# Optimization experiments

Hardware: AMD Instinct MI355X
Metric: run time of the kernel (lower is better)

## Reference

```python
import jax, jax.numpy as jnp
import numpy as np

ALLOWED_SPANLEN = 7
NEG = -10000.0      # init value for logalpha, matching torch fill_(-10000.)
MASK_NEG = -1e9     # additive mask for out-of-window span starts


def setup_inputs() -> dict:
    key = jax.random.key(0)
    k1, k2 = jax.random.split(key)
    B, L, T = 16, 128, 11  # batch, sent_len, tagset_size (9 tags + START + STOP)
    scores = jax.random.normal(k1, (B, L, L, T, T), dtype=jnp.float32)
    # mask holds sentence lengths in [L//2, L] (used as gather index into logalpha)
    mask = jax.random.randint(k2, (B,), L // 2, L + 1, dtype=jnp.int32)
    return {"scores": scores, "mask": mask}


def reference(scores, mask):
    """Semi-CRF forward DP (get_logloss_denominator).

    scores: (B, L, L, T, T) -- scores[b, j, i, y_prev, y] is the score of a span
            [j, i] labeled y, with previous segment label y_prev.
    mask:   (B,) sentence lengths.
    """
    B, L, _, T, _ = scores.shape
    K = ALLOWED_SPANLEN
    start_id, stop_id = T - 1, T - 2

    alpha0 = jnp.full((B, L + 1, T), NEG, dtype=scores.dtype)
    alpha0 = alpha0.at[:, 0, start_id].set(0.0)

    # Re-index scores by span-end position so scan can stream one end per step.
    scores_by_end = jnp.moveaxis(scores, 2, 0)  # (L_end, B, L_start, T, T)
    offs = jnp.arange(K)

    def step(alpha, xs):
        i, sc = xs                # i in [1..L]; sc: (B, L, Tprev, Tcur), end = i-1
        js = i - K + offs         # candidate span starts: [i-K, i-1]
        valid = (js >= 0)[None, :, None, None]
        jsc = jnp.clip(js, 0, L - 1)
        a_w = jnp.take(alpha, jsc, axis=1)   # (B, K, Tprev)
        s_w = jnp.take(sc, jsc, axis=1)      # (B, K, Tprev, Tcur)
        t = jnp.where(valid, s_w + a_w[:, :, :, None], MASK_NEG)
        new = jax.nn.logsumexp(t, axis=(1, 2))           # (B, Tcur)
        alpha = jax.lax.dynamic_update_slice(alpha, new[:, None, :], (0, i, 0))
        return alpha, None

    alpha, _ = jax.lax.scan(step, alpha0, (jnp.arange(1, L + 1), scores_by_end))
    # gather logalpha at the sentence-length position for each batch element
    final = alpha[jnp.arange(B), mask, :]                # (B, T)
    return final[:, stop_id].sum()
```

## Files before the change

kernel.cpp:

```cpp
#include <hip/hip_runtime.h>
#include <math.h>

#define LL 128
#define TT 11
#define NP 121
#define KK 7
#define GS 20
#define SPW 240

#define LOG2E 1.4426950408889634f
#define LN2   0.6931471805599453f

__device__ __forceinline__ float fast_exp2(float x) { return __builtin_amdgcn_exp2f(x); }
__device__ __forceinline__ float fast_log2(float x) { return __builtin_amdgcn_logf(x); }
#if __has_builtin(__builtin_amdgcn_rcpf)
__device__ __forceinline__ float fast_rcp(float x) { return __builtin_amdgcn_rcpf(x); }
#else
__device__ __forceinline__ float fast_rcp(float x) { return 1.0f / x; }
#endif
__device__ __forceinline__ float rfl(float x) {
    return __int_as_float(__builtin_amdgcn_readfirstlane(__float_as_int(x)));
}
__device__ __forceinline__ void cfence() { __builtin_amdgcn_wave_barrier(); }

__global__ __launch_bounds__(64, 1) void hscrf_fused(const float* __restrict__ scores,
                                                     const int* __restrict__ mask,
                                                     float* __restrict__ out,
                                                     int n_batch)
{
    const int l = threadIdx.x;
    const int b = blockIdx.x;
    if (b >= n_batch) return;

    __shared__ __align__(64) float sp[SPW];

    const int o1  = l + 64;
    const int o1c = (o1 < NP) ? o1 : 0;
    const int y0 = l / TT,   yp0 = l % TT;
    const int y1 = o1c / TT, yp1 = o1c % TT;
    const int e0 = yp0 * TT + y0;
    const int e1 = yp1 * TT + y1;
    const int i0w = y0 * GS + yp0;
    const int i1w = (o1 < NP) ? (y1 * GS + yp1) : (220 + (l - 57));

    if (l < TT) sp[l * GS + 11] = 0.0f;

    const int mb = mask[b];
    const float* sb = scores + (size_t)b * (size_t)(LL * LL * NP);

    float rA0[KK], rA1[KK], rB0[KK], rB1[KK];
    float rC0[KK], rC1[KK], rD0[KK], rD1[KK];
    float eX0[KK], eX1[KK], eY0[KK], eY1[KK];

    auto load_pane = [&](int p, float (&L0)[KK], float (&L1)[KK]) {
#pragma unroll
        for (int k = 0; k < KK; ++k) {
            const int j  = p - KK + k;
            const int jc = j < 0 ? 0 : j;
            const size_t base = ((size_t)jc * LL + (size_t)(p - 1)) * NP;
            L0[k] = sb[base + e0];
            L1[k] = sb[base + e1];
        }
    };

    auto convert = [&](int p, const float (&R0)[KK], const float (&R1)[KK],
                       float (&D0)[KK], float (&D1)[KK]) {
#pragma unroll
        for (int k = 0; k < KK; ++k) {
            const float ev0 = fast_exp2(R0[k] * LOG2E);
            const float ev1 = fast_exp2(R1[k] * LOG2E);
            const bool ok = (p - KK + k) >= 0;
            D0[k] = ok ? ev0 : 0.0f;
            D1[k] = ok ? ev1 : 0.0f;
        }
    };

    float W0[KK], W1[KK];
#pragma unroll
    for (int k = 0; k < KK; ++k) { W0[k] = 0.0f; W1[k] = 0.0f; }
    W0[KK - 1] = (yp0 == TT - 1) ? 1.0f : 0.0f;
    W1[KK - 1] = (yp1 == TT - 1) ? 1.0f : 0.0f;

    float Cc = 0.0f;
    float saved = 0.0f;

    load_pane(1, rA0, rA1); load_pane(2, rB0, rB1);
    load_pane(3, rC0, rC1); load_pane(4, rD0, rD1);
    convert(1, rA0, rA1, eX0, eX1);
    convert(2, rB0, rB1, eY0, eY1);

    auto body = [&](int i, bool do_load, bool do_conv,
                    float (&EC0)[KK], float (&EC1)[KK],
                    float (&LT0)[KK], float (&LT1)[KK],
                    float (&RS0)[KK], float (&RS1)[KK]) {
        float p0 = fmaf(EC0[0], W0[0], EC0[1] * W0[1]);
        float q0 = fmaf(EC0[2], W0[2], EC0[3] * W0[3]);
        float u0 = fmaf(EC0[4], W0[4], EC0[5] * W0[5]);
        float s0 = (p0 + q0) + fmaf(EC0[6], W0[6], u0);
        float p1 = fmaf(EC1[0], W1[0], EC1[1] * W1[1]);
        float q1 = fmaf(EC1[2], W1[2], EC1[3] * W1[3]);
        float u1 = fmaf(EC1[4], W1[4], EC1[5] * W1[5]);
        float s1 = (p1 + q1) + fmaf(EC1[6], W1[6], u1);
        sp[i0w] = s0;
        sp[i1w] = s1;

        cfence();

        const float4 qa0 = *(const float4*)(sp + yp0 * GS);
        const float4 qb0 = *(const float4*)(sp + yp0 * GS + 4);
        const float4 qc0 = *(const float4*)(sp + yp0 * GS + 8);
        const float4 qa1 = *(const float4*)(sp + yp1 * GS);
        const float4 qb1 = *(const float4*)(sp + yp1 * GS + 4);
        const float4 qc1 = *(const float4*)(sp + yp1 * GS + 8);

        if (do_load) load_pane(i + 4, LT0, LT1);
        if (do_conv) convert(i + 2, RS0, RS1, EC0, EC1);

        const float SA = (((qa0.x + qa0.y) + (qa0.z + qa0.w)) +
                          ((qb0.x + qb0.y) + (qb0.z + qb0.w))) +
                         ((qc0.x + qc0.y) + (qc0.z + qc0.w));
        const float SB = (((qa1.x + qa1.y) + (qa1.z + qa1.w)) +
                          ((qb1.x + qb1.y) + (qb1.z + qb1.w))) +
                         ((qc1.x + qc1.y) + (qc1.z + qc1.w));

        const float s0u = rfl(SA);
        const float r = fast_rcp(s0u);

        saved = (i == mb) ? Cc + fast_log2(SA) : saved;
        Cc += fast_log2(s0u);

#pragma unroll
        for (int k = 0; k < KK - 1; ++k) { W0[k] = W0[k + 1] * r; W1[k] = W1[k + 1] * r; }
        W0[KK - 1] = SA * r;
        W1[KK - 1] = SB * r;

        cfence();
    };

    for (int i = 1; i <= LL - 4; i += 4) {
        body(i,     true, true, eX0, eX1, rA0, rA1, rC0, rC1);
        body(i + 1, true, true, eY0, eY1, rB0, rB1, rD0, rD1);
        body(i + 2, true, true, eX0, eX1, rC0, rC1, rA0, rA1);
        body(i + 3, true, true, eY0, eY1, rD0, rD1, rB0, rB1);
    }
    body(LL - 3, false, true,  eX0, eX1, rA0, rA1, rC0, rC1);
    body(LL - 2, false, true,  eY0, eY1, rB0, rB1, rD0, rD1);
    body(LL - 1, false, false, eX0, eX1, rA0, rA1, rA0, rA1);
    body(LL,     false, false, eY0, eY1, rB0, rB1, rB0, rB1);

    if (l == TT - 2) {
        atomicAdd(out, saved * LN2);
    }
}

extern "C" void kernel_launch(void* const* d_in, const int* in_sizes, int n_in,
                              void* d_out, int out_size, void* d_ws, size_t ws_size,
                              hipStream_t stream) {
    const float* scores = (const float*)d_in[0];
    const int*   mask   = (const int*)d_in[1];
    float* out = (float*)d_out;
    const int B = in_sizes[1];

    hipMemsetAsync(out, 0, sizeof(float) * out_size, stream);

    (void)d_ws; (void)ws_size;

    hscrf_fused<<<B, 64, 0, stream>>>(scores, mask, out, B);
}
```

Before: 210.4 us.

## Stream score panes into an LDS ring via async global-to-LDS loads

New measurement: 248.0 us. +17.9%, slower.

```diff
diff --git a/kernel.cpp b/kernel.cpp
--- a/kernel.cpp
+++ b/kernel.cpp
@@ -7,9 +7,13 @@
 #define KK 7
 #define GS 20
 #define SPW 240
+#define NSLOT 8
 
 #define LOG2E 1.4426950408889634f
 #define LN2   0.6931471805599453f
+
+typedef const __attribute__((address_space(1))) unsigned int* gas_t;
+typedef __attribute__((address_space(3)))       unsigned int* las_t;
 
 __device__ __forceinline__ float fast_exp2(float x) { return __builtin_amdgcn_exp2f(x); }
 __device__ __forceinline__ float fast_log2(float x) { return __builtin_amdgcn_logf(x); }
@@ -23,15 +27,27 @@
 }
 __device__ __forceinline__ void cfence() { __builtin_amdgcn_wave_barrier(); }
 
-__global__ __launch_bounds__(64, 1) void hscrf_fused(const float* __restrict__ scores,
-                                                     const int* __restrict__ mask,
-                                                     float* __restrict__ out,
-                                                     int n_batch)
+__device__ __forceinline__ void vmwait(int n) {
+    switch (n) {
+        case 0:  asm volatile("s_waitcnt vmcnt(0)"  ::: "memory"); break;
+        case 7:  asm volatile("s_waitcnt vmcnt(7)"  ::: "memory"); break;
+        case 14: asm volatile("s_waitcnt vmcnt(14)" ::: "memory"); break;
+        case 21: asm volatile("s_waitcnt vmcnt(21)" ::: "memory"); break;
+        case 28: asm volatile("s_waitcnt vmcnt(28)" ::: "memory"); break;
+        default: break;
+    }
+}
+
+__global__ __launch_bounds__(64, 1) void hscrf_fused2(const float* __restrict__ scores,
+                                                      const int* __restrict__ mask,
+                                                      float* __restrict__ out,
+                                                      int n_batch)
 {
     const int l = threadIdx.x;
     const int b = blockIdx.x;
     if (b >= n_batch) return;
 
+    __shared__ __align__(64) float ring[NSLOT][KK][256];
     __shared__ __align__(64) float sp[SPW];
 
     const int o1  = l + 64;
@@ -39,39 +55,44 @@
     const int y0 = l / TT,   yp0 = l % TT;
     const int y1 = o1c / TT, yp1 = o1c % TT;
     const int e0 = yp0 * TT + y0;
-    const int e1 = yp1 * TT + y1;
+    const int e1 = o1c % TT * TT + o1c / TT;
+    const int f0 = e0;
+    const int f1 = (e1 == 120) ? 123 : e1;
     const int i0w = y0 * GS + yp0;
     const int i1w = (o1 < NP) ? (y1 * GS + yp1) : (220 + (l - 57));
 
     if (l < TT) sp[l * GS + 11] = 0.0f;
 
     const int mb = mask[b];
-    const float* sb = scores + (size_t)b * (size_t)(LL * LL * NP);
+    const float* sb = scores + (size_t)b * (size_t)(LL * (size_t)LL * NP);
 
-    float rA0[KK], rA1[KK], rB0[KK], rB1[KK];
-    float rC0[KK], rC1[KK], rD0[KK], rD1[KK];
-    float eX0[KK], eX1[KK], eY0[KK], eY1[KK];
+    const int src_off = (l < 30) ? l * 16 : ((l == 30) ? 468 : 0);
 
-    auto load_pane = [&](int p, float (&L0)[KK], float (&L1)[KK]) {
+    auto dma_pane = [&](int p) {
+        const int slot = p & (NSLOT - 1);
+        const int pi = p - 1;
 #pragma unroll
         for (int k = 0; k < KK; ++k) {
             const int j  = p - KK + k;
             const int jc = j < 0 ? 0 : j;
-            const size_t base = ((size_t)jc * LL + (size_t)(p - 1)) * NP;
-            L0[k] = sb[base + e0];
-            L1[k] = sb[base + e1];
+            const float* slice = sb + ((size_t)jc * LL + (size_t)pi) * NP;
+            __builtin_amdgcn_global_load_lds(
+                (gas_t)((const char*)slice + src_off),
+                (las_t)&ring[slot][k][0], 16, 0, 0);
         }
     };
 
-    auto convert = [&](int p, const float (&R0)[KK], const float (&R1)[KK],
-                       float (&D0)[KK], float (&D1)[KK]) {
+    auto convert = [&](int p, float (&D0)[KK], float (&D1)[KK]) {
+        const int slot = p & (NSLOT - 1);
 #pragma unroll
         for (int k = 0; k < KK; ++k) {
-            const float ev0 = fast_exp2(R0[k] * LOG2E);
-            const float ev1 = fast_exp2(R1[k] * LOG2E);
+            const float r0 = ring[slot][k][f0];
+            const float r1 = ring[slot][k][f1];
+            const float v0 = fast_exp2(r0 * LOG2E);
+            const float v1 = fast_exp2(r1 * LOG2E);
             const bool ok = (p - KK + k) >= 0;
-            D0[k] = ok ? ev0 : 0.0f;
-            D1[k] = ok ? ev1 : 0.0f;
+            D0[k] = ok ? v0 : 0.0f;
+            D1[k] = ok ? v1 : 0.0f;
         }
     };
 
@@ -84,15 +105,15 @@
     float Cc = 0.0f;
     float saved = 0.0f;
 
-    load_pane(1, rA0, rA1); load_pane(2, rB0, rB1);
-    load_pane(3, rC0, rC1); load_pane(4, rD0, rD1);
-    convert(1, rA0, rA1, eX0, eX1);
-    convert(2, rB0, rB1, eY0, eY1);
+    float eX0[KK], eX1[KK], eY0[KK], eY1[KK];
 
-    auto body = [&](int i, bool do_load, bool do_conv,
+    dma_pane(1); dma_pane(2); dma_pane(3); dma_pane(4); dma_pane(5);
+    vmwait(28);
+    convert(1, eX0, eX1);
+
+    auto body = [&](int i, bool do_load, int vmw, bool do_conv,
                     float (&EC0)[KK], float (&EC1)[KK],
-                    float (&LT0)[KK], float (&LT1)[KK],
-                    float (&RS0)[KK], float (&RS1)[KK]) {
+                    float (&EN0)[KK], float (&EN1)[KK]) {
         float p0 = fmaf(EC0[0], W0[0], EC0[1] * W0[1]);
         float q0 = fmaf(EC0[2], W0[2], EC0[3] * W0[3]);
         float u0 = fmaf(EC0[4], W0[4], EC0[5] * W0[5]);
@@ -113,8 +134,9 @@
         const float4 qb1 = *(const float4*)(sp + yp1 * GS + 4);
         const float4 qc1 = *(const float4*)(sp + yp1 * GS + 8);
 
-        if (do_load) load_pane(i + 4, LT0, LT1);
-        if (do_conv) convert(i + 2, RS0, RS1, EC0, EC1);
+        if (do_load) dma_pane(i + 5);
+        vmwait(vmw);
+        if (do_conv) convert(i + 1, EN0, EN1);
 
         const float SA = (((qa0.x + qa0.y) + (qa0.z + qa0.w)) +
                           ((qb0.x + qb0.y) + (qb0.z + qb0.w))) +
@@ -137,16 +159,16 @@
         cfence();
     };
 
-    for (int i = 1; i <= LL - 4; i += 4) {
-        body(i,     true, true, eX0, eX1, rA0, rA1, rC0, rC1);
-        body(i + 1, true, true, eY0, eY1, rB0, rB1, rD0, rD1);
-        body(i + 2, true, true, eX0, eX1, rC0, rC1, rA0, rA1);
-        body(i + 3, true, true, eY0, eY1, rD0, rD1, rB0, rB1);
+    for (int i = 1; i <= 121; i += 2) {
+        body(i,     true, 28, true, eX0, eX1, eY0, eY1);
+        body(i + 1, true, 28, true, eY0, eY1, eX0, eX1);
     }
-    body(LL - 3, false, true,  eX0, eX1, rA0, rA1, rC0, rC1);
-    body(LL - 2, false, true,  eY0, eY1, rB0, rB1, rD0, rD1);
-    body(LL - 1, false, false, eX0, eX1, rA0, rA1, rA0, rA1);
-    body(LL,     false, false, eY0, eY1, rB0, rB1, rB0, rB1);
+    body(123, true,  28, true,  eX0, eX1, eY0, eY1);
+    body(124, false, 21, true,  eY0, eY1, eX0, eX1);
+    body(125, false, 14, true,  eX0, eX1, eY0, eY1);
+    body(126, false,  7, true,  eY0, eY1, eX0, eX1);
+    body(127, false,  0, true,  eX0, eX1, eY0, eY1);
+    body(128, false, -1, false, eY0, eY1, eX0, eX1);
 
     if (l == TT - 2) {
         atomicAdd(out, saved * LN2);
@@ -165,5 +187,5 @@
 
     (void)d_ws; (void)ws_size;
 
-    hscrf_fused<<<B, 64, 0, stream>>>(scores, mask, out, B);
+    hscrf_fused2<<<B, 64, 0, stream>>>(scores, mask, out, B);
 }
```

## Split loading and DP into producer/consumer waves with an LDS ring buffer

Applied to the files above, without the earlier changes.

Measured after the change: 200.7 us. -4.6%, faster.

```diff
diff --git a/kernel.cpp b/kernel.cpp
--- a/kernel.cpp
+++ b/kernel.cpp
@@ -7,6 +7,8 @@
 #define KK 7
 #define GS 20
 #define SPW 240
+#define NSLOT 8
+#define PANEF 1024
 
 #define LOG2E 1.4426950408889634f
 #define LN2   0.6931471805599453f
@@ -22,134 +24,190 @@
     return __int_as_float(__builtin_amdgcn_readfirstlane(__float_as_int(x)));
 }
 __device__ __forceinline__ void cfence() { __builtin_amdgcn_wave_barrier(); }
-
-__global__ __launch_bounds__(64, 1) void hscrf_fused(const float* __restrict__ scores,
-                                                     const int* __restrict__ mask,
-                                                     float* __restrict__ out,
-                                                     int n_batch)
+#define VMWAIT28() asm volatile("s_waitcnt vmcnt(28)" ::: "memory")
+#define VMWAIT0()  asm volatile("s_waitcnt vmcnt(0)"  ::: "memory")
+#define LGKM0()    asm volatile("s_waitcnt lgkmcnt(0)" ::: "memory")
+
+__device__ __forceinline__ void block_sync() {
+    asm volatile("" ::: "memory");
+    __builtin_amdgcn_s_barrier();
+    asm volatile("" ::: "memory");
+}
+
+__global__ __launch_bounds__(128, 1) void hscrf_pc(const float* __restrict__ scores,
+                                                   const int* __restrict__ mask,
+                                                   float* __restrict__ out,
+                                                   int n_batch)
 {
-    const int l = threadIdx.x;
-    const int b = blockIdx.x;
+    const int tid = threadIdx.x;
+    const int l   = tid & 63;
+    const int wid = tid >> 6;
+    const int b   = blockIdx.x;
     if (b >= n_batch) return;
 
+    __shared__ __align__(64) float ring[NSLOT][PANEF];
     __shared__ __align__(64) float sp[SPW];
 
-    const int o1  = l + 64;
-    const int o1c = (o1 < NP) ? o1 : 0;
-    const int y0 = l / TT,   yp0 = l % TT;
-    const int y1 = o1c / TT, yp1 = o1c % TT;
-    const int e0 = yp0 * TT + y0;
-    const int e1 = yp1 * TT + y1;
-    const int i0w = y0 * GS + yp0;
-    const int i1w = (o1 < NP) ? (y1 * GS + yp1) : (220 + (l - 57));
-
-    if (l < TT) sp[l * GS + 11] = 0.0f;
-
-    const int mb = mask[b];
-    const float* sb = scores + (size_t)b * (size_t)(LL * LL * NP);
-
-    float rA0[KK], rA1[KK], rB0[KK], rB1[KK];
-    float rC0[KK], rC1[KK], rD0[KK], rD1[KK];
-    float eX0[KK], eX1[KK], eY0[KK], eY1[KK];
-
-    auto load_pane = [&](int p, float (&L0)[KK], float (&L1)[KK]) {
-#pragma unroll
-        for (int k = 0; k < KK; ++k) {
-            const int j  = p - KK + k;
-            const int jc = j < 0 ? 0 : j;
-            const size_t base = ((size_t)jc * LL + (size_t)(p - 1)) * NP;
-            L0[k] = sb[base + e0];
-            L1[k] = sb[base + e1];
+    const float* sb = scores + (size_t)b * (size_t)(LL * (size_t)LL * NP);
+
+    if (wid == 1) {
+        const int o1  = l + 64;
+        const bool v1 = (o1 < NP);
+        const int o1c = v1 ? o1 : 0;
+        const int e0 = (l % TT) * TT + (l / TT);
+        const int e1 = (o1c % TT) * TT + (o1c / TT);
+
+        float XA0[KK], XA1[KK], XB0[KK], XB1[KK];
+        float YA0[KK], YA1[KK], YB0[KK], YB1[KK];
+
+        auto issue2 = [&](int p, float (&a0)[KK], float (&a1)[KK],
+                          float (&c0)[KK], float (&c1)[KK]) {
+#pragma unroll
+            for (int k = 0; k < KK; ++k) {
+                const int j = p - KK + k; const int jc = j < 0 ? 0 : j;
+                const float* s0 = sb + ((size_t)jc * LL + (size_t)(p - 1)) * NP;
+                a0[k] = s0[e0]; a1[k] = s0[e1];
+            }
+#pragma unroll
+            for (int k = 0; k < KK; ++k) {
+                const int j = p + 1 - KK + k; const int jc = j < 0 ? 0 : j;
+                const float* s1 = sb + ((size_t)jc * LL + (size_t)p) * NP;
+                c0[k] = s1[e0]; c1[k] = s1[e1];
+            }
+        };
+
+        auto conv1 = [&](int p, const float (&a0)[KK], const float (&a1)[KK]) {
+            const int slot = p & (NSLOT - 1);
+            float v0[8], v1[8];
+#pragma unroll
+            for (int k = 0; k < KK; ++k) {
+                const bool ok = (p - KK + k) >= 0;
+                const float t0 = fast_exp2(a0[k] * LOG2E);
+                const float t1 = fast_exp2(a1[k] * LOG2E);
+                v0[k] = ok ? t0 : 0.0f;
+                v1[k] = (ok && v1) ? t1 : 0.0f;
+            }
+            v0[7] = 0.0f; v1[7] = 0.0f;
+            float4* dst = (float4*)&ring[slot][0];
+            dst[l]       = make_float4(v0[0], v0[1], v0[2], v0[3]);
+            dst[128 + l] = make_float4(v0[4], v0[5], v0[6], v0[7]);
+            dst[64 + l]  = make_float4(v1[0], v1[1], v1[2], v1[3]);
+            dst[192 + l] = make_float4(v1[4], v1[5], v1[6], v1[7]);
+        };
+
+        issue2(1, XA0, XA1, XB0, XB1);
+        issue2(3, YA0, YA1, YB0, YB1);
+        VMWAIT28();
+        conv1(1, XA0, XA1); conv1(2, XB0, XB1);
+        issue2(5, XA0, XA1, XB0, XB1);
+        VMWAIT28();
+        conv1(3, YA0, YA1); conv1(4, YB0, YB1);
+        LGKM0(); block_sync();
+
+        for (int t = 1; t <= 59; t += 2) {
+            issue2(2 * t + 5, YA0, YA1, YB0, YB1);
+            VMWAIT28();
+            conv1(2 * t + 3, XA0, XA1); conv1(2 * t + 4, XB0, XB1);
+            LGKM0(); block_sync();
+            issue2(2 * t + 7, XA0, XA1, XB0, XB1);
+            VMWAIT28();
+            conv1(2 * t + 5, YA0, YA1); conv1(2 * t + 6, YB0, YB1);
+            LGKM0(); block_sync();
         }
-    };
-
-    auto convert = [&](int p, const float (&R0)[KK], const float (&R1)[KK],
-                       float (&D0)[KK], float (&D1)[KK]) {
-#pragma unroll
-        for (int k = 0; k < KK; ++k) {
-            const float ev0 = fast_exp2(R0[k] * LOG2E);
-            const float ev1 = fast_exp2(R1[k] * LOG2E);
-            const bool ok = (p - KK + k) >= 0;
-            D0[k] = ok ? ev0 : 0.0f;
-            D1[k] = ok ? ev1 : 0.0f;
+        issue2(127, YA0, YA1, YB0, YB1);
+        VMWAIT28();
+        conv1(125, XA0, XA1); conv1(126, XB0, XB1);
+        LGKM0(); block_sync();
+        VMWAIT0();
+        conv1(127, YA0, YA1); conv1(128, YB0, YB1);
+        LGKM0(); block_sync();
+        block_sync();
+        block_sync();
+    } else {
+        const int o1  = l + 64;
+        const int o1c = (o1 < NP) ? o1 : 0;
+        const int y0 = l / TT,   yp0 = l % TT;
+        const int y1 = o1c / TT, yp1 = o1c % TT;
+        const int i0w = y0 * GS + yp0;
+        const int i1w = (o1 < NP) ? (y1 * GS + yp1) : (220 + (l - 57));
+
+        if (l < TT) sp[l * GS + 11] = 0.0f;
+
+        const int mb = mask[b];
+
+        float W0[KK], W1[KK];
+#pragma unroll
+        for (int k = 0; k < KK; ++k) { W0[k] = 0.0f; W1[k] = 0.0f; }
+        W0[KK - 1] = (yp0 == TT - 1) ? 1.0f : 0.0f;
+        W1[KK - 1] = (yp1 == TT - 1) ? 1.0f : 0.0f;
+
+        float Cc = 0.0f;
+        float saved = 0.0f;
+
+        block_sync();
+
+        const float4* ep1 = (const float4*)&ring[1][0];
+        float4 ea0 = ep1[l],      ea1 = ep1[128 + l];
+        float4 eb0 = ep1[64 + l], eb1 = ep1[192 + l];
+
+        auto body = [&](int i) {
+            float p0 = fmaf(ea0.x, W0[0], ea0.y * W0[1]);
+            float q0 = fmaf(ea0.z, W0[2], ea0.w * W0[3]);
+            float u0 = fmaf(ea1.x, W0[4], ea1.y * W0[5]);
+            float s0 = (p0 + q0) + fmaf(ea1.z, W0[6], u0);
+            float p1 = fmaf(eb0.x, W1[0], eb0.y * W1[1]);
+            float q1 = fmaf(eb0.z, W1[2], eb0.w * W1[3]);
+            float u1 = fmaf(eb1.x, W1[4], eb1.y * W1[5]);
+            float s1 = (p1 + q1) + fmaf(eb1.z, W1[6], u1);
+            sp[i0w] = s0;
+            sp[i1w] = s1;
+
+            cfence();
+
+            const float4 qa0 = *(const float4*)(sp + yp0 * GS);
+            const float4 qb0 = *(const float4*)(sp + yp0 * GS + 4);
+            const float4 qc0 = *(const float4*)(sp + yp0 * GS + 8);
+            const float4 qa1 = *(const float4*)(sp + yp1 * GS);
+            const float4 qb1 = *(const float4*)(sp + yp1 * GS + 4);
+            const float4 qc1 = *(const float4*)(sp + yp1 * GS + 8);
+
+            const int ns = (i + 1) & (NSLOT - 1);
+            const float4* ep = (const float4*)&ring[ns][0];
+            const float4 na0 = ep[l],      na1 = ep[128 + l];
+            const float4 nb0 = ep[64 + l], nb1 = ep[192 + l];
+
+            const float SA = (((qa0.x + qa0.y) + (qa0.z + qa0.w)) +
+                              ((qb0.x + qb0.y) + (qb0.z + qb0.w))) +
+                             ((qc0.x + qc0.y) + (qc0.z + qc0.w));
+            const float SB = (((qa1.x + qa1.y) + (qa1.z + qa1.w)) +
+                              ((qb1.x + qb1.y) + (qb1.z + qb1.w))) +
+                             ((qc1.x + qc1.y) + (qc1.z + qc1.w));
+
+            const float s0u = rfl(SA);
+            const float r = fast_rcp(s0u);
+
+            saved = (i == mb) ? Cc + fast_log2(SA) : saved;
+            Cc += fast_log2(s0u);
+
+#pragma unroll
+            for (int k = 0; k < KK - 1; ++k) { W0[k] = W0[k + 1] * r; W1[k] = W1[k + 1] * r; }
+            W0[KK - 1] = SA * r;
+            W1[KK - 1] = SB * r;
+
+            ea0 = na0; ea1 = na1; eb0 = nb0; eb1 = nb1;
+
+            cfence();
+        };
+
+        for (int i = 1; i <= LL; i += 2) {
+            body(i);
+            body(i + 1);
+            block_sync();
         }
-    };
-
-    float W0[KK], W1[KK];
-#pragma unroll
-    for (int k = 0; k < KK; ++k) { W0[k] = 0.0f; W1[k] = 0.0f; }
-    W0[KK - 1] = (yp0 == TT - 1) ? 1.0f : 0.0f;
-    W1[KK - 1] = (yp1 == TT - 1) ? 1.0f : 0.0f;
-
-    float Cc = 0.0f;
-    float saved = 0.0f;
-
-    load_pane(1, rA0, rA1); load_pane(2, rB0, rB1);
-    load_pane(3, rC0, rC1); load_pane(4, rD0, rD1);
-    convert(1, rA0, rA1, eX0, eX1);
-    convert(2, rB0, rB1, eY0, eY1);
-
-    auto body = [&](int i, bool do_load, bool do_conv,
-                    float (&EC0)[KK], float (&EC1)[KK],
-                    float (&LT0)[KK], float (&LT1)[KK],
-                    float (&RS0)[KK], float (&RS1)[KK]) {
-        float p0 = fmaf(EC0[0], W0[0], EC0[1] * W0[1]);
-        float q0 = fmaf(EC0[2], W0[2], EC0[3] * W0[3]);
-        float u0 = fmaf(EC0[4], W0[4], EC0[5] * W0[5]);
-        float s0 = (p0 + q0) + fmaf(EC0[6], W0[6], u0);
-        float p1 = fmaf(EC1[0], W1[0], EC1[1] * W1[1]);
-        float q1 = fmaf(EC1[2], W1[2], EC1[3] * W1[3]);
-        float u1 = fmaf(EC1[4], W1[4], EC1[5] * W1[5]);
-        float s1 = (p1 + q1) + fmaf(EC1[6], W1[6], u1);
-        sp[i0w] = s0;
-        sp[i1w] = s1;
-
-        cfence();
-
-        const float4 qa0 = *(const float4*)(sp + yp0 * GS);
-        const float4 qb0 = *(const float4*)(sp + yp0 * GS + 4);
-        const float4 qc0 = *(const float4*)(sp + yp0 * GS + 8);
-        const float4 qa1 = *(const float4*)(sp + yp1 * GS);
-        const float4 qb1 = *(const float4*)(sp + yp1 * GS + 4);
-        const float4 qc1 = *(const float4*)(sp + yp1 * GS + 8);
-
-        if (do_load) load_pane(i + 4, LT0, LT1);
-        if (do_conv) convert(i + 2, RS0, RS1, EC0, EC1);
-
-        const float SA = (((qa0.x + qa0.y) + (qa0.z + qa0.w)) +
-                          ((qb0.x + qb0.y) + (qb0.z + qb0.w))) +
-                         ((qc0.x + qc0.y) + (qc0.z + qc0.w));
-        const float SB = (((qa1.x + qa1.y) + (qa1.z + qa1.w)) +
-                          ((qb1.x + qb1.y) + (qb1.z + qb1.w))) +
-                         ((qc1.x + qc1.y) + (qc1.z + qc1.w));
-
-        const float s0u = rfl(SA);
-        const float r = fast_rcp(s0u);
-
-        saved = (i == mb) ? Cc + fast_log2(SA) : saved;
-        Cc += fast_log2(s0u);
-
-#pragma unroll
-        for (int k = 0; k < KK - 1; ++k) { W0[k] = W0[k + 1] * r; W1[k] = W1[k + 1] * r; }
-        W0[KK - 1] = SA * r;
-        W1[KK - 1] = SB * r;
-
-        cfence();
-    };
-
-    for (int i = 1; i <= LL - 4; i += 4) {
-        body(i,     true, true, eX0, eX1, rA0, rA1, rC0, rC1);
-        body(i + 1, true, true, eY0, eY1, rB0, rB1, rD0, rD1);
-        body(i + 2, true, true, eX0, eX1, rC0, rC1, rA0, rA1);
-        body(i + 3, true, true, eY0, eY1, rD0, rD1, rB0, rB1);
-    }
-    body(LL - 3, false, true,  eX0, eX1, rA0, rA1, rC0, rC1);
-    body(LL - 2, false, true,  eY0, eY1, rB0, rB1, rD0, rD1);
-    body(LL - 1, false, false, eX0, eX1, rA0, rA1, rA0, rA1);
-    body(LL,     false, false, eY0, eY1, rB0, rB1, rB0, rB1);
-
-    if (l == TT - 2) {
-        atomicAdd(out, saved * LN2);
+
+        if (l == TT - 2) {
+            atomicAdd(out, saved * LN2);
+        }
     }
 }
 
@@ -165,5 +223,5 @@
 
     (void)d_ws; (void)ws_size;
 
-    hscrf_fused<<<B, 64, 0, stream>>>(scores, mask, out, B);
-}
+    hscrf_pc<<<B, 128, 0, stream>>>(scores, mask, out, B);
+}
```
